# Kernel tuning notes

Measured on AMD Instinct MI355X. Metric: run time of the kernel, lower is better.

## Reference

```python
import jax, jax.numpy as jnp
import numpy as np

EMBED_SIZE = 1024
HEADS = 16
HEAD_DIM = EMBED_SIZE // HEADS


def setup_inputs() -> dict:
    key = jax.random.key(0)
    ks = jax.random.split(key, 9)
    N, L = 2, 2048
    inv = 1.0 / np.sqrt(HEAD_DIM)
    return {
        "values": jax.random.normal(ks[0], (N, L, EMBED_SIZE), dtype=jnp.float32),
        "keys": jax.random.normal(ks[1], (N, L, EMBED_SIZE), dtype=jnp.float32),
        "query": jax.random.normal(ks[2], (N, L, EMBED_SIZE), dtype=jnp.float32),
        "mask": jnp.ones((N, 1, 1, L), dtype=jnp.int32),
        # per-head projections: a single head_dim x head_dim weight shared across heads
        "Wv": jax.random.normal(ks[3], (HEAD_DIM, HEAD_DIM), dtype=jnp.float32) * inv,
        "Wk": jax.random.normal(ks[4], (HEAD_DIM, HEAD_DIM), dtype=jnp.float32) * inv,
        "Wq": jax.random.normal(ks[5], (HEAD_DIM, HEAD_DIM), dtype=jnp.float32) * inv,
        "Wo": jax.random.normal(ks[6], (EMBED_SIZE, EMBED_SIZE), dtype=jnp.float32) / np.sqrt(EMBED_SIZE),
        "bo": jnp.zeros((EMBED_SIZE,), dtype=jnp.float32),
    }


def reference(values, keys, query, mask, Wv, Wk, Wq, Wo, bo):
    N, q_len, E = query.shape
    k_len = keys.shape[1]
    v_len = values.shape[1]
    H, D = HEADS, HEAD_DIM

    v = values.reshape(N, v_len, H, D)
    k = keys.reshape(N, k_len, H, D)
    q = query.reshape(N, q_len, H, D)

    # nn.Linear(head_dim, head_dim, bias=False): y = x @ W.T, same W for every head
    v = jnp.einsum("nlhd,ed->nlhe", v, Wv)
    k = jnp.einsum("nlhd,ed->nlhe", k, Wk)
    q = jnp.einsum("nqhd,ed->nqhe", q, Wq)

    # full [N, H, Q, K] score matrix, as in the original
    energy = jnp.einsum("nqhd,nkhd->nhqk", q, k)
    energy = jnp.where(mask == 0, jnp.float32(-1e20), energy)

    # NOTE: scale is sqrt(embed_size), not sqrt(head_dim), applied after masking
    attention = jax.nn.softmax(energy / jnp.sqrt(jnp.float32(E)), axis=3)

    out = jnp.einsum("nhql,nlhd->nqhd", attention, v).reshape(N, q_len, H * D)
    out = out @ Wo.T + bo
    return out
```

## Files before the change

kernel.cpp:

```cpp
#include <hip/hip_runtime.h>

#define HEADS 16
#define HDIM 64
#define EMB 1024
#define SEQ 2048
#define NBATCH 2

typedef short short8 __attribute__((ext_vector_type(8)));
typedef float f32x4 __attribute__((ext_vector_type(4)));
typedef float f32x16 __attribute__((ext_vector_type(16)));

__device__ __forceinline__ unsigned short f2bf(float f) {
  unsigned u = __builtin_bit_cast(unsigned, f);
  u += 0x7fffu + ((u >> 16) & 1u);
  return (unsigned short)(u >> 16);
}

__device__ __forceinline__ unsigned cvtpk(float lo, float hi) {
  unsigned r;
  asm("v_cvt_pk_bf16_f32 %0, %1, %2" : "=v"(r) : "v"(lo), "v"(hi));
  return r;
}

__device__ __forceinline__ void swap32(unsigned& a, unsigned& b) {
  asm("v_permlane32_swap_b32 %0, %1" : "+v"(a), "+v"(b));
}

__global__ __launch_bounds__(256) void prep_kernel(
    const float* __restrict__ src, unsigned short* __restrict__ dst,
    const int* __restrict__ mask, float* __restrict__ biasf,
    int* __restrict__ flags, const float* __restrict__ Wq,
    const float* __restrict__ Wk, const float* __restrict__ Wv,
    unsigned short* __restrict__ wqkv, float qscale) {
  int b = blockIdx.x;
  int t = threadIdx.x;
  if (b < 1024) {
    int i = (b * 256 + t) * 4;
    float4 v = *(const float4*)(src + i);
    uint2 pk;
    pk.x = (unsigned)f2bf(v.x) | ((unsigned)f2bf(v.y) << 16);
    pk.y = (unsigned)f2bf(v.z) | ((unsigned)f2bf(v.w) << 16);
    *(uint2*)(dst + i) = pk;
  } else if (b < 1028) {
    int i = (b - 1024) * 1024 + t * 4;
    int4 m = *(const int4*)(mask + i);
    float4 o;
    o.x = m.x ? 0.0f : -1e30f;
    o.y = m.y ? 0.0f : -1e30f;
    o.z = m.z ? 0.0f : -1e30f;
    o.w = m.w ? 0.0f : -1e30f;
    *(float4*)(biasf + i) = o;
  } else if (b == 1028) {
    if (t < 64) {
      int n = t >> 5, tile = t & 31;
      const int* mp = mask + n * SEQ + tile * 64;
      int anyz = 0;
#pragma unroll
      for (int i = 0; i < 16; ++i) {
        int4 m = *(const int4*)(mp + i * 4);
        anyz |= (!m.x) | (!m.y) | (!m.z) | (!m.w);
      }
      flags[t] = anyz;
    }
  } else {
    int j = (b - 1029) * 1024 + t * 4;
    const float* s;
    int off = j;
    float sc = 1.0f;
    if (j < 4096) { s = Wq; sc = qscale; }
    else if (j < 8192) { s = Wk; off = j - 4096; }
    else { s = Wv; off = j - 8192; }
    float4 v = *(const float4*)(s + off);
    uint2 pk;
    pk.x = (unsigned)f2bf(v.x * sc) | ((unsigned)f2bf(v.y * sc) << 16);
    pk.y = (unsigned)f2bf(v.z * sc) | ((unsigned)f2bf(v.w * sc) << 16);
    *(uint2*)(wqkv + j) = pk;
  }
}

__global__ __launch_bounds__(256) void proj_kernel(
    const float* __restrict__ q_in, const float* __restrict__ k_in,
    const float* __restrict__ v_in, const unsigned short* __restrict__ wqkv,
    unsigned short* __restrict__ qp, unsigned short* __restrict__ kp,
    unsigned short* __restrict__ vt) {
  int t = threadIdx.x;
  int w = t >> 6, lane = t & 63;
  int l5 = lane & 31, hi = lane >> 5;

  __shared__ uint4 Wl[1536];
#pragma unroll
  for (int i = 0; i < 6; ++i) {
    int idx = i * 256 + t;
    int row = idx >> 3, c8 = idx & 7;
    Wl[row * 8 + (c8 ^ (row & 7))] = *(const uint4*)(wqkv + idx * 8);
  }
  __syncthreads();

  int d = (int)blockIdx.x;
  int work = (d & 7) * 192 + (d >> 3);
  int u = work * 4 + w;
  int rest = u / 3;
  int tensor = u - rest * 3;
  int l32 = rest & 63, h = (rest >> 6) & 15, n = rest >> 10;
  int lbase = l32 * 32;

  const float* x = tensor == 0 ? q_in : (tensor == 1 ? k_in : v_in);
  const float* xr = x + ((size_t)(n * SEQ + lbase + l5) * HEADS + h) * HDIM + hi * 8;

  short8 xf[4];
#pragma unroll
  for (int ds = 0; ds < 4; ++ds) {
    float4 a = *(const float4*)(xr + ds * 16);
    float4 bb = *(const float4*)(xr + ds * 16 + 4);
    uint4 u4;
    u4.x = cvtpk(a.x, a.y);
    u4.y = cvtpk(a.z, a.w);
    u4.z = cvtpk(bb.x, bb.y);
    u4.w = cvtpk(bb.z, bb.w);
    xf[ds] = __builtin_bit_cast(short8, u4);
  }

  const int rsw = l5 & 7;
  int wrow0 = tensor * 64 + l5;
  int wrow1 = wrow0 + 32;
  f32x16 acc0 = {}, acc1 = {};

  if (tensor < 2) {
#pragma unroll
    for (int ds = 0; ds < 4; ++ds) {
      short8 w0 = __builtin_bit_cast(short8, Wl[wrow0 * 8 + ((ds * 2 + hi) ^ rsw)]);
      short8 w1 = __builtin_bit_cast(short8, Wl[wrow1 * 8 + ((ds * 2 + hi) ^ rsw)]);
      acc0 = __builtin_amdgcn_mfma_f32_32x32x16_bf16(w0, xf[ds], acc0, 0, 0, 0);
      acc1 = __builtin_amdgcn_mfma_f32_32x32x16_bf16(w1, xf[ds], acc1, 0, 0, 0);
    }
    unsigned short* orow = (tensor == 0 ? qp : kp) +
        ((size_t)(n * HEADS + h) * SEQ + lbase + l5) * HDIM + hi * 4;
#pragma unroll
    for (int g = 0; g < 4; ++g) {
      uint2 o0, o1;
      o0.x = cvtpk(acc0[g * 4 + 0], acc0[g * 4 + 1]);
      o0.y = cvtpk(acc0[g * 4 + 2], acc0[g * 4 + 3]);
      o1.x = cvtpk(acc1[g * 4 + 0], acc1[g * 4 + 1]);
      o1.y = cvtpk(acc1[g * 4 + 2], acc1[g * 4 + 3]);
      *(uint2*)(orow + g * 8) = o0;
      *(uint2*)(orow + 32 + g * 8) = o1;
    }
  } else {
#pragma unroll
    for (int ds = 0; ds < 4; ++ds) {
      short8 w0 = __builtin_bit_cast(short8, Wl[wrow0 * 8 + ((ds * 2 + hi) ^ rsw)]);
      short8 w1 = __builtin_bit_cast(short8, Wl[wrow1 * 8 + ((ds * 2 + hi) ^ rsw)]);
      acc0 = __builtin_amdgcn_mfma_f32_32x32x16_bf16(xf[ds], w0, acc0, 0, 0, 0);
      acc1 = __builtin_amdgcn_mfma_f32_32x32x16_bf16(xf[ds], w1, acc1, 0, 0, 0);
    }
    unsigned short* vb = vt + (size_t)(n * HEADS + h) * HDIM * SEQ;
    unsigned short* r0 = vb + (size_t)l5 * SEQ + lbase + hi * 4;
    unsigned short* r1 = vb + (size_t)(32 + l5) * SEQ + lbase + hi * 4;
#pragma unroll
    for (int g = 0; g < 4; ++g) {
      uint2 o0, o1;
      o0.x = cvtpk(acc0[g * 4 + 0], acc0[g * 4 + 1]);
      o0.y = cvtpk(acc0[g * 4 + 2], acc0[g * 4 + 3]);
      o1.x = cvtpk(acc1[g * 4 + 0], acc1[g * 4 + 1]);
      o1.y = cvtpk(acc1[g * 4 + 2], acc1[g * 4 + 3]);
      *(uint2*)(r0 + g * 8) = o0;
      *(uint2*)(r1 + g * 8) = o1;
    }
  }
}

__global__ __launch_bounds__(512, 4) void attn_kernel(
    const unsigned short* __restrict__ qp, const unsigned short* __restrict__ kp,
    const unsigned short* __restrict__ vt, const float* __restrict__ biasf,
    const int* __restrict__ flags, unsigned short* __restrict__ ao) {
  int t = threadIdx.x;
  int w = t >> 6;
  int lane = t & 63;
  int l5 = lane & 31, hi = lane >> 5;
  int ks = w >> 2;
  int wq = w & 3;

  int d = (int)blockIdx.x;
  int work = (d & 7) * 64 + (d >> 3);
  int qs = work & 15;
  int h = (work >> 4) & 15;
  int n = work >> 8;
  int qw = qs * 128 + wq * 32;

  size_t slab = (size_t)(n * HEADS + h);
  const unsigned short* Qb = qp + slab * SEQ * HDIM;
  const unsigned short* Kb = kp + slab * SEQ * HDIM;
  const unsigned short* Vb = vt + slab * (size_t)HDIM * SEQ;
  const float* biasp = biasf + n * SEQ;
  const int* flagp = flags + n * 32;

  __shared__ uint4 Kl[2][2][512];
  __shared__ uint4 Vl[2][2][512];

  int tt = t & 255;

  auto STAGE = [&](int buf, int kb) {
#pragma unroll
    for (int i = 0; i < 2; ++i) {
      int idx = i * 256 + tt;
      int row = idx >> 3;
      int c8 = (idx & 7) ^ (row & 7);
      const unsigned short* gk = Kb + (size_t)(kb + row) * HDIM + c8 * 8;
      const unsigned short* gv = Vb + (size_t)row * SEQ + kb + c8 * 8;
      __builtin_amdgcn_global_load_lds(
          (const __attribute__((address_space(1))) unsigned*)gk,
          (__attribute__((address_space(3))) unsigned*)&Kl[ks][buf][i * 256 + (tt >> 6) * 64],
          16, 0, 0);
      __builtin_amdgcn_global_load_lds(
          (const __attribute__((address_space(1))) unsigned*)gv,
          (__attribute__((address_space(3))) unsigned*)&Vl[ks][buf][i * 256 + (tt >> 6) * 64],
          16, 0, 0);
    }
  };

  short8 bq[4];
  {
    const unsigned short* qrow = Qb + (size_t)(qw + l5) * HDIM + hi * 8;
#pragma unroll
    for (int dstep = 0; dstep < 4; ++dstep)
      bq[dstep] = __builtin_bit_cast(short8, *(const uint4*)(qrow + dstep * 16));
  }

  f32x16 acc0 = {}, acc1 = {};
  float lrun = 0.0f;
  const int rsw = l5 & 7;
  const float FM = 8.0f;
  int k0 = ks * (SEQ / 2);

  STAGE(0, k0);
  int cur = 0;

#pragma unroll 1
  for (int t8 = 0; t8 < SEQ / 2 / 64; ++t8) {
    int kb = k0 + t8 * 64;
    __syncthreads();
    if (t8 + 1 < SEQ / 2 / 64) STAGE(cur ^ 1, kb + 64);

    f32x16 s0 = {}, s1 = {};
    __builtin_amdgcn_s_setprio(1);
#pragma unroll
    for (int dstep = 0; dstep < 4; ++dstep) {
      short8 kf0 = __builtin_bit_cast(short8, Kl[ks][cur][l5 * 8 + ((dstep * 2 + hi) ^ rsw)]);
      short8 kf1 = __builtin_bit_cast(short8, Kl[ks][cur][256 + l5 * 8 + ((dstep * 2 + hi) ^ rsw)]);
      s0 = __builtin_amdgcn_mfma_f32_32x32x16_bf16(kf0, bq[dstep], s0, 0, 0, 0);
      s1 = __builtin_amdgcn_mfma_f32_32x32x16_bf16(kf1, bq[dstep], s1, 0, 0, 0);
    }
    __builtin_amdgcn_s_setprio(0);

    if (flagp[kb >> 6]) {
#pragma unroll
      for (int g = 0; g < 4; ++g) {
        f32x4 b0 = *(const f32x4*)(biasp + kb + g * 8 + hi * 4);
        f32x4 b1 = *(const f32x4*)(biasp + kb + 32 + g * 8 + hi * 4);
#pragma unroll
        for (int i = 0; i < 4; ++i) {
          s0[g * 4 + i] += b0[i];
          s1[g * 4 + i] += b1[i];
        }
      }
    }

    float ps = 0.0f;
    unsigned wv[16];
#pragma unroll
    for (int i = 0; i < 8; ++i) {
      float p0 = exp2f(s0[2 * i] - FM);
      float p1 = exp2f(s0[2 * i + 1] - FM);
      ps += p0 + p1;
      wv[i] = cvtpk(p0, p1);
    }
#pragma unroll
    for (int i = 0; i < 8; ++i) {
      float p0 = exp2f(s1[2 * i] - FM);
      float p1 = exp2f(s1[2 * i + 1] - FM);
      ps += p0 + p1;
      wv[8 + i] = cvtpk(p0, p1);
    }
    lrun += ps;

    short8 pf[4];
#pragma unroll
    for (int kt = 0; kt < 2; ++kt) {
#pragma unroll
      for (int s = 0; s < 2; ++s) {
        unsigned a = wv[kt * 8 + s * 4 + 0], c = wv[kt * 8 + s * 4 + 2];
        unsigned b = wv[kt * 8 + s * 4 + 1], dd = wv[kt * 8 + s * 4 + 3];
        swap32(a, c);
        swap32(b, dd);
        uint4 u = {a, b, c, dd};
        pf[kt * 2 + s] = __builtin_bit_cast(short8, u);
      }
    }

    __builtin_amdgcn_s_setprio(1);
#pragma unroll
    for (int ks4 = 0; ks4 < 4; ++ks4) {
      short8 v0 = __builtin_bit_cast(short8, Vl[ks][cur][l5 * 8 + ((ks4 * 2 + hi) ^ rsw)]);
      short8 v1 = __builtin_bit_cast(short8, Vl[ks][cur][256 + l5 * 8 + ((ks4 * 2 + hi) ^ rsw)]);
      acc0 = __builtin_amdgcn_mfma_f32_32x32x16_bf16(v0, pf[ks4], acc0, 0, 0, 0);
      acc1 = __builtin_amdgcn_mfma_f32_32x32x16_bf16(v1, pf[ks4], acc1, 0, 0, 0);
    }
    __builtin_amdgcn_s_setprio(0);
    cur ^= 1;
  }

  __syncthreads();
  float* cb = (float*)&Kl[0][0][0];
  float* lb = (float*)&Vl[0][0][0];
  if (w >= 4) {
    float* dst = cb + (w - 4) * 2048;
#pragma unroll
    for (int r = 0; r < 16; ++r) {
      dst[r * 64 + lane] = acc0[r];
      dst[(r + 16) * 64 + lane] = acc1[r];
    }
    lb[(w - 4) * 64 + lane] = lrun;
  }
  __syncthreads();
  if (w < 4) {
    const float* src = cb + w * 2048;
#pragma unroll
    for (int r = 0; r < 16; ++r) {
      acc0[r] += src[r * 64 + lane];
      acc1[r] += src[(r + 16) * 64 + lane];
    }
    lrun += lb[w * 64 + lane];
    float lt = lrun + __shfl_xor(lrun, 32, 64);
    float inv = 1.0f / lt;

    unsigned short* obase =
        ao + ((size_t)(n * SEQ + qw + l5)) * EMB + h * HDIM + hi * 4;
#pragma unroll
    for (int g = 0; g < 4; ++g) {
      uint2 o0, o1;
      o0.x = cvtpk(acc0[g * 4 + 0] * inv, acc0[g * 4 + 1] * inv);
      o0.y = cvtpk(acc0[g * 4 + 2] * inv, acc0[g * 4 + 3] * inv);
      o1.x = cvtpk(acc1[g * 4 + 0] * inv, acc1[g * 4 + 1] * inv);
      o1.y = cvtpk(acc1[g * 4 + 2] * inv, acc1[g * 4 + 3] * inv);
      *(uint2*)(obase + g * 8) = o0;
      *(uint2*)(obase + 32 + g * 8) = o1;
    }
  }
}

__global__ __launch_bounds__(256) void gemm_bt_kernel(
    const unsigned short* __restrict__ Ag, const unsigned short* __restrict__ Bg,
    const float* __restrict__ bias, float* __restrict__ Cm) {
  int t = threadIdx.x;
  int lane = t & 63, w = t >> 6;
  int lr = lane & 15, lg = lane >> 4;
  int wr = w >> 1, wc = w & 1;

  int d = (int)blockIdx.x;
  int work = (d & 7) * 64 + (d >> 3);
  int bx = work & 15, by = work >> 4;
  int m0 = by * 128, n0 = bx * 64;

  __shared__ uint4 Al[2][1024];
  __shared__ uint4 Bl[2][512];

  int wu = __builtin_amdgcn_readfirstlane(w);

  auto STAGE_G = [&](int buf, int kt) {
#pragma unroll
    for (int i = 0; i < 4; ++i) {
      int idx = i * 256 + t;
      int row = idx >> 3, c8 = (idx & 7) ^ (row & 7);
      __builtin_amdgcn_global_load_lds(
          (const __attribute__((address_space(1))) unsigned*)(
              Ag + (size_t)(m0 + row) * EMB + kt + c8 * 8),
          (__attribute__((address_space(3))) unsigned*)&Al[buf][i * 256 + wu * 64],
          16, 0, 0);
    }
#pragma unroll
    for (int i = 0; i < 2; ++i) {
      int idx = i * 256 + t;
      int row = idx >> 3, c8 = (idx & 7) ^ (row & 7);
      __builtin_amdgcn_global_load_lds(
          (const __attribute__((address_space(1))) unsigned*)(
              Bg + (size_t)(n0 + row) * EMB + kt + c8 * 8),
          (__attribute__((address_space(3))) unsigned*)&Bl[buf][i * 256 + wu * 64],
          16, 0, 0);
    }
  };

  f32x4 zero = {0.0f, 0.0f, 0.0f, 0.0f};
  f32x4 acc[4][2];
#pragma unroll
  for (int mt = 0; mt < 4; ++mt)
#pragma unroll
    for (int nt = 0; nt < 2; ++nt) acc[mt][nt] = zero;

  auto COMP = [&](int buf) __attribute__((always_inline)) {
#pragma unroll
    for (int kk = 0; kk < 2; ++kk) {
      short8 af[4], bfr[2];
#pragma unroll
      for (int mt = 0; mt < 4; ++mt) {
        int row = wr * 64 + mt * 16 + lr;
        af[mt] = __builtin_bit_cast(short8, Al[buf][(row * 8 + kk * 4 + lg) ^ (row & 7)]);
      }
#pragma unroll
      for (int nt = 0; nt < 2; ++nt) {
        int row = wc * 32 + nt * 16 + lr;
        bfr[nt] = __builtin_bit_cast(short8, Bl[buf][(row * 8 + kk * 4 + lg) ^ (row & 7)]);
      }
#pragma unroll
      for (int mt = 0; mt < 4; ++mt)
#pragma unroll
        for (int nt = 0; nt < 2; ++nt)
          acc[mt][nt] = __builtin_amdgcn_mfma_f32_16x16x32_bf16(af[mt], bfr[nt],
                                                                acc[mt][nt], 0, 0, 0);
    }
  };

  STAGE_G(0, 0);
#pragma unroll 1
  for (int kt = 0; kt < EMB; kt += 128) {
    __syncthreads();
    STAGE_G(1, kt + 64);
    COMP(0);
    __syncthreads();
    if (kt + 128 < EMB) STAGE_G(0, kt + 128);
    COMP(1);
  }

#pragma unroll
  for (int nt = 0; nt < 2; ++nt) {
    int col = n0 + wc * 32 + nt * 16 + lr;
    float bv = bias[col];
#pragma unroll
    for (int mt = 0; mt < 4; ++mt) {
#pragma unroll
      for (int i = 0; i < 4; ++i) {
        int rowm = m0 + wr * 64 + mt * 16 + lg * 4 + i;
        Cm[(size_t)rowm * EMB + col] = acc[mt][nt][i] + bv;
      }
    }
  }
}

extern "C" void kernel_launch(void* const* d_in, const int* in_sizes, int n_in,
                              void* d_out, int out_size, void* d_ws, size_t ws_size,
                              hipStream_t stream) {
  const float* values = (const float*)d_in[0];
  const float* keys   = (const float*)d_in[1];
  const float* query  = (const float*)d_in[2];
  const int*   mask   = (const int*)d_in[3];
  const float* Wv     = (const float*)d_in[4];
  const float* Wk     = (const float*)d_in[5];
  const float* Wq     = (const float*)d_in[6];
  const float* Wo     = (const float*)d_in[7];
  const float* bo     = (const float*)d_in[8];
  float* out = (float*)d_out;

  const size_t slab = (size_t)NBATCH * HEADS * SEQ * HDIM;
  unsigned short* qp  = (unsigned short*)d_ws;
  unsigned short* kp  = qp + slab;
  unsigned short* vt  = kp + slab;
  unsigned short* ao  = vt + slab;
  unsigned short* wob = ao + slab;
  float* biasf = (float*)(wob + (size_t)EMB * EMB);
  int* flags = (int*)(biasf + NBATCH * SEQ);
  unsigned short* wqkv = (unsigned short*)(flags + 64);

  float qscale = 1.4426950408889634f / 32.0f;

  prep_kernel<<<dim3(1041), 256, 0, stream>>>(Wo, wob, mask, biasf, flags,
                                              Wq, Wk, Wv, wqkv, qscale);
  proj_kernel<<<dim3(1536), 256, 0, stream>>>(query, keys, values, wqkv, qp, kp, vt);
  attn_kernel<<<dim3((SEQ / 128) * HEADS * NBATCH), 512, 0, stream>>>(
      qp, kp, vt, biasf, flags, ao);
  gemm_bt_kernel<<<dim3(512), 256, 0, stream>>>(ao, wob, bo, out);
}
```

Measured before the change: 107.3 us.

## Split attention key range across four wave groups, dropping double-buffered staging

The attention block grows from 512 to 1024 threads, so four key-split groups each cover a quarter of the sequence instead of two groups covering halves. The double-buffered K/V LDS prefetch becomes a single buffer that is loaded and then synchronized at the top of every iteration, with a second barrier at the end. The final reduction becomes a two-level tree through LDS with a separate row-sum buffer. This adds parallelism and per-CU waves, but load latency is no longer hidden by prefetch and the 1024-thread blocks may limit occupancy and register budget.

```diff
diff --git a/kernel.cpp b/kernel.cpp
--- a/kernel.cpp
+++ b/kernel.cpp
@@ -169,7 +169,7 @@
   }
 }
 
-__global__ __launch_bounds__(512, 4) void attn_kernel(
+__global__ __launch_bounds__(1024, 8) void attn_kernel(
     const unsigned short* __restrict__ qp, const unsigned short* __restrict__ kp,
     const unsigned short* __restrict__ vt, const float* __restrict__ biasf,
     const int* __restrict__ flags, unsigned short* __restrict__ ao) {
@@ -194,12 +194,13 @@
   const float* biasp = biasf + n * SEQ;
   const int* flagp = flags + n * 32;
 
-  __shared__ uint4 Kl[2][2][512];
-  __shared__ uint4 Vl[2][2][512];
+  __shared__ uint4 Kl[4][512];
+  __shared__ uint4 Vl[4][512];
+  __shared__ float lml[12 * 64];
 
   int tt = t & 255;
 
-  auto STAGE = [&](int buf, int kb) {
+  auto STAGE = [&](int kb) {
 #pragma unroll
     for (int i = 0; i < 2; ++i) {
       int idx = i * 256 + tt;
@@ -209,11 +210,11 @@
       const unsigned short* gv = Vb + (size_t)row * SEQ + kb + c8 * 8;
       __builtin_amdgcn_global_load_lds(
           (const __attribute__((address_space(1))) unsigned*)gk,
-          (__attribute__((address_space(3))) unsigned*)&Kl[ks][buf][i * 256 + (tt >> 6) * 64],
+          (__attribute__((address_space(3))) unsigned*)&Kl[ks][i * 256 + (tt >> 6) * 64],
           16, 0, 0);
       __builtin_amdgcn_global_load_lds(
           (const __attribute__((address_space(1))) unsigned*)gv,
-          (__attribute__((address_space(3))) unsigned*)&Vl[ks][buf][i * 256 + (tt >> 6) * 64],
+          (__attribute__((address_space(3))) unsigned*)&Vl[ks][i * 256 + (tt >> 6) * 64],
           16, 0, 0);
     }
   };
@@ -230,23 +231,20 @@
   float lrun = 0.0f;
   const int rsw = l5 & 7;
   const float FM = 8.0f;
-  int k0 = ks * (SEQ / 2);
-
-  STAGE(0, k0);
-  int cur = 0;
+  int k0 = ks * (SEQ / 4);
 
 #pragma unroll 1
-  for (int t8 = 0; t8 < SEQ / 2 / 64; ++t8) {
+  for (int t8 = 0; t8 < SEQ / 4 / 64; ++t8) {
     int kb = k0 + t8 * 64;
+    STAGE(kb);
     __syncthreads();
-    if (t8 + 1 < SEQ / 2 / 64) STAGE(cur ^ 1, kb + 64);
 
     f32x16 s0 = {}, s1 = {};
     __builtin_amdgcn_s_setprio(1);
 #pragma unroll
     for (int dstep = 0; dstep < 4; ++dstep) {
-      short8 kf0 = __builtin_bit_cast(short8, Kl[ks][cur][l5 * 8 + ((dstep * 2 + hi) ^ rsw)]);
-      short8 kf1 = __builtin_bit_cast(short8, Kl[ks][cur][256 + l5 * 8 + ((dstep * 2 + hi) ^ rsw)]);
+      short8 kf0 = __builtin_bit_cast(short8, Kl[ks][l5 * 8 + ((dstep * 2 + hi) ^ rsw)]);
+      short8 kf1 = __builtin_bit_cast(short8, Kl[ks][256 + l5 * 8 + ((dstep * 2 + hi) ^ rsw)]);
       s0 = __builtin_amdgcn_mfma_f32_32x32x16_bf16(kf0, bq[dstep], s0, 0, 0, 0);
       s1 = __builtin_amdgcn_mfma_f32_32x32x16_bf16(kf1, bq[dstep], s1, 0, 0, 0);
     }
@@ -300,36 +298,55 @@
     __builtin_amdgcn_s_setprio(1);
 #pragma unroll
     for (int ks4 = 0; ks4 < 4; ++ks4) {
-      short8 v0 = __builtin_bit_cast(short8, Vl[ks][cur][l5 * 8 + ((ks4 * 2 + hi) ^ rsw)]);
-      short8 v1 = __builtin_bit_cast(short8, Vl[ks][cur][256 + l5 * 8 + ((ks4 * 2 + hi) ^ rsw)]);
+      short8 v0 = __builtin_bit_cast(short8, Vl[ks][l5 * 8 + ((ks4 * 2 + hi) ^ rsw)]);
+      short8 v1 = __builtin_bit_cast(short8, Vl[ks][256 + l5 * 8 + ((ks4 * 2 + hi) ^ rsw)]);
       acc0 = __builtin_amdgcn_mfma_f32_32x32x16_bf16(v0, pf[ks4], acc0, 0, 0, 0);
       acc1 = __builtin_amdgcn_mfma_f32_32x32x16_bf16(v1, pf[ks4], acc1, 0, 0, 0);
     }
     __builtin_amdgcn_s_setprio(0);
-    cur ^= 1;
-  }
-
-  __syncthreads();
-  float* cb = (float*)&Kl[0][0][0];
-  float* lb = (float*)&Vl[0][0][0];
-  if (w >= 4) {
-    float* dst = cb + (w - 4) * 2048;
+    __syncthreads();
+  }
+
+  if (w >= 8) {
+    float* dst = (w < 12) ? ((float*)Kl + (size_t)(w - 8) * 2048)
+                          : ((float*)Vl + (size_t)(w - 12) * 2048);
 #pragma unroll
     for (int r = 0; r < 16; ++r) {
       dst[r * 64 + lane] = acc0[r];
       dst[(r + 16) * 64 + lane] = acc1[r];
     }
-    lb[(w - 4) * 64 + lane] = lrun;
+    lml[(w - 8) * 64 + lane] = lrun;
   }
   __syncthreads();
-  if (w < 4) {
-    const float* src = cb + w * 2048;
+  if (w < 8) {
+    const float* src = (w < 4) ? ((const float*)Kl + (size_t)w * 2048)
+                               : ((const float*)Vl + (size_t)(w - 4) * 2048);
 #pragma unroll
     for (int r = 0; r < 16; ++r) {
       acc0[r] += src[r * 64 + lane];
       acc1[r] += src[(r + 16) * 64 + lane];
     }
-    lrun += lb[w * 64 + lane];
+    lrun += lml[w * 64 + lane];
+  }
+  __syncthreads();
+  if (w >= 4 && w < 8) {
+    float* dst = (float*)Kl + (size_t)(w - 4) * 2048;
+#pragma unroll
+    for (int r = 0; r < 16; ++r) {
+      dst[r * 64 + lane] = acc0[r];
+      dst[(r + 16) * 64 + lane] = acc1[r];
+    }
+    lml[(8 + (w - 4)) * 64 + lane] = lrun;
+  }
+  __syncthreads();
+  if (w < 4) {
+    const float* src = (const float*)Kl + (size_t)w * 2048;
+#pragma unroll
+    for (int r = 0; r < 16; ++r) {
+      acc0[r] += src[r * 64 + lane];
+      acc1[r] += src[(r + 16) * 64 + lane];
+    }
+    lrun += lml[(8 + w) * 64 + lane];
     float lt = lrun + __shfl_xor(lrun, 32, 64);
     float inv = 1.0f / lt;
 
@@ -474,7 +491,7 @@
   prep_kernel<<<dim3(1041), 256, 0, stream>>>(Wo, wob, mask, biasf, flags,
                                               Wq, Wk, Wv, wqkv, qscale);
   proj_kernel<<<dim3(1536), 256, 0, stream>>>(query, keys, values, wqkv, qp, kp, vt);
-  attn_kernel<<<dim3((SEQ / 128) * HEADS * NBATCH), 512, 0, stream>>>(
+  attn_kernel<<<dim3((SEQ / 128) * HEADS * NBATCH), 1024, 0, stream>>>(
       qp, kp, vt, biasf, flags, ao);
   gemm_bt_kernel<<<dim3(512), 256, 0, stream>>>(ao, wob, bo, out);
 }
```

Result: slower. 334.7 us (+211.9%).
